# Performance work log

Hardware: AMD Instinct MI355X
Metric: run time of the kernel (lower is better)

The kernel has to match this reference:

```python
import jax, jax.numpy as jnp
import numpy as np

BS, N, F, R, OUT = 8, 512, 512, 16, 512
ALPHA = 0.2

def setup_inputs() -> dict:
    key = jax.random.key(0)
    ks = jax.random.split(key, 16)
    w = lambda k, shp: (jax.random.normal(k, shp, dtype=jnp.float32) * 0.05)
    return {
        'x_ori': jax.random.normal(ks[0], (BS, N, F), dtype=jnp.float32),
        'x': jax.random.normal(ks[1], (BS, N, F), dtype=jnp.float32),
        'c': jax.random.normal(ks[2], (BS, 1, F), dtype=jnp.float32),
        'adj': jax.random.randint(ks[3], (BS, N, N, R), 0, 2, dtype=jnp.int32),
        'Wfc': w(ks[4], (F, F)),
        'Wdc': w(ks[5], (F, F)),
        'Wqv': w(ks[6], (2 * F, F)),
        'Wkv': w(ks[7], (2 * F, F)),
        'Wqc': w(ks[8], (F, F)),
        'Wkc': w(ks[9], (F, F)),
        'Wa': w(ks[10], (2 * F, R)),
        'Wu': w(ks[11], (2 * F, OUT)),
    }

def reference(x_ori, x, c, adj, Wfc, Wdc, Wqv, Wkv, Wqc, Wkc, Wa, Wu):
    # relation-context modulation vector m: [bs,1,F]
    m = jnp.matmul(jax.nn.elu(jnp.matmul(c, Wfc)), Wdc)
    nodes = jnp.concatenate([x, x_ori], axis=2)          # [bs,N,2F]
    xq = jnp.matmul(nodes, Wqv) * jnp.matmul(m, Wqc)     # [bs,N,F]
    xk = jnp.matmul(nodes, Wkv) * jnp.matmul(m, Wkc)     # [bs,N,F]
    # scores[b,i,j,r] = leakyrelu(xq_i . Wa[:F,r] + xk_j . Wa[F:,r])
    # (equivalent to cat([xq_i,xk_j]) @ Wa without materializing [bs,N,N,2F])
    sq = jnp.matmul(xq, Wa[:F])                          # [bs,N,R]
    sk = jnp.matmul(xk, Wa[F:])                          # [bs,N,R]
    scores = jax.nn.leaky_relu(sq[:, :, None, :] + sk[:, None, :, :], ALPHA)
    adj_f = adj.astype(scores.dtype)                     # [bs,N,N,R]
    s = jnp.sum(scores * adj_f, axis=3)                  # [bs,N,N]
    mask = jnp.sum(adj_f, axis=3) > 0
    attn = jax.nn.softmax(jnp.where(mask, s, jnp.float32(-9e15)), axis=2)
    new_x = jnp.matmul(attn, x)                          # [bs,N,F]
    return jnp.matmul(jnp.concatenate([x, new_x], axis=2), Wu)
```

## Files before the change

### kernel.cpp

```cpp
#include <hip/hip_runtime.h>
#include <hip/hip_bf16.h>
#include <cstddef>
#include <cstdint>

static constexpr int BSZ  = 8;
static constexpr int NN   = 512;
static constexpr int FF   = 512;
static constexpr int RR   = 16;
static constexpr int TWOF = 1024;

typedef __attribute__((ext_vector_type(8))) short short8;
typedef __attribute__((ext_vector_type(4))) float f32x4;

__device__ __forceinline__ ushort bf16_bits(float v) {
    union { __hip_bfloat16 h; ushort u; } cvt;
    cvt.h = __float2bfloat16(v);
    return cvt.u;
}

static constexpr size_t OFF_TB     = 0;
static constexpr size_t OFF_MB     = 16384;
static constexpr size_t OFF_MQ     = 32768;
static constexpr size_t OFF_MK     = 49152;
static constexpr size_t OFF_SQ     = 65536;
static constexpr size_t OFF_SK     = 327680;
static constexpr size_t OFF_WQET   = 589824;
static constexpr size_t OFF_WKET   = 851968;
static constexpr size_t OFF_XBF    = 5308416;
static constexpr size_t OFF_XTBF   = 9502720;
static constexpr size_t OFF_XORIBF = 13697024;
static constexpr size_t OFF_NEWXBF = 17891328;
static constexpr size_t OFF_WUT    = 22085632;
static constexpr size_t OFF_MASK   = 23134208;

__global__ __launch_bounds__(256) void k_prep(
    const float* __restrict__ x_ori, const float* __restrict__ x,
    const float* __restrict__ c, const float* __restrict__ Wfc,
    const float* __restrict__ Wu, const int* __restrict__ adj,
    ushort* __restrict__ xori_bf, ushort* __restrict__ x_bf,
    ushort* __restrict__ xT_bf, ushort* __restrict__ WuT,
    float* __restrict__ tb, ushort* __restrict__ masks)
{
    int blk = blockIdx.x;
    int t = threadIdx.x;
    if (blk < 1024) {
        int idx = blk * 256 + t;
        float4 a = ((const float4*)x_ori)[idx * 2];
        float4 b = ((const float4*)x_ori)[idx * 2 + 1];
        uint4 s;
        s.x = (uint)bf16_bits(a.x) | ((uint)bf16_bits(a.y) << 16);
        s.y = (uint)bf16_bits(a.z) | ((uint)bf16_bits(a.w) << 16);
        s.z = (uint)bf16_bits(b.x) | ((uint)bf16_bits(b.y) << 16);
        s.w = (uint)bf16_bits(b.z) | ((uint)bf16_bits(b.w) << 16);
        ((uint4*)xori_bf)[idx] = s;
    } else if (blk < 3072) {
        __shared__ float tile[32][33];
        int bb = blk - 1024;
        int f0 = (bb & 15) * 32, i0 = ((bb >> 4) & 15) * 32, b = bb >> 8;
        int c2 = (t & 15) * 2, r = t >> 4;
#pragma unroll
        for (int rr = 0; rr < 32; rr += 16) {
            int i = i0 + r + rr;
            const float* xp = &x[((size_t)b * NN + i) * FF + f0 + c2];
            float v0 = xp[0], v1 = xp[1];
            tile[r + rr][c2] = v0;
            tile[r + rr][c2 + 1] = v1;
            *(uint*)&x_bf[((size_t)b * NN + i) * FF + f0 + c2] =
                (uint)bf16_bits(v0) | ((uint)bf16_bits(v1) << 16);
        }
        __syncthreads();
#pragma unroll
        for (int ff = 0; ff < 32; ff += 16) {
            int f = f0 + r + ff;
            *(uint*)&xT_bf[((size_t)b * FF + f) * NN + i0 + c2] =
                (uint)bf16_bits(tile[c2][r + ff]) |
                ((uint)bf16_bits(tile[c2 + 1][r + ff]) << 16);
        }
    } else if (blk < 3584) {
        __shared__ float tile2[32][33];
        int bb = blk - 3072;
        int f0 = (bb & 31) * 32, o0 = (bb >> 5) * 32;
        int cc = t & 31, r0 = t >> 5;
#pragma unroll
        for (int rr = 0; rr < 32; rr += 8)
            tile2[r0 + rr][cc] = Wu[(size_t)(f0 + r0 + rr) * FF + o0 + cc];
        __syncthreads();
#pragma unroll
        for (int rr = 0; rr < 32; rr += 8)
            WuT[(size_t)(o0 + r0 + rr) * TWOF + f0 + cc] = bf16_bits(tile2[cc][r0 + rr]);
    } else if (blk < 3712) {
        __shared__ float red1[8][32];
        int bb = blk - 3584;
        int b = bb >> 4, f0 = (bb & 15) * 32;
        int f = t & 31, kq = t >> 5;
        const float* vb = c + (size_t)b * FF;
        float acc = 0.f;
        int ks = kq * 64;
#pragma unroll 8
        for (int k = ks; k < ks + 64; ++k)
            acc = fmaf(vb[k], Wfc[(size_t)k * FF + f0 + f], acc);
        red1[kq][f] = acc;
        __syncthreads();
        if (kq == 0) {
            acc += red1[1][f] + red1[2][f] + red1[3][f] + red1[4][f] +
                   red1[5][f] + red1[6][f] + red1[7][f];
            tb[(size_t)b * FF + f0 + f] = (acc > 0.f) ? acc : expm1f(acc);
        }
    } else {
        int pb = (blk - 3712) * 1024;
        const int4* a4 = (const int4*)adj;
        uint* m32 = (uint*)masks;
#pragma unroll 8
        for (int i = 0; i < 16; ++i) {
            size_t g4 = (size_t)pb * 4 + (size_t)i * 256 + t;
            int4 v = a4[g4];
            uint bits = (uint)v.x | ((uint)v.y << 1) | ((uint)v.z << 2) | ((uint)v.w << 3);
            uint mp = bits << ((t & 3) * 4);
            mp |= (uint)__shfl_xor((int)mp, 1, 64);
            mp |= (uint)__shfl_xor((int)mp, 2, 64);
            uint hi = (uint)__shfl_xor((int)mp, 4, 64);
            if ((t & 7) == 0)
                m32[(size_t)pb / 2 + i * 32 + (t >> 3)] = (mp & 0xFFFFu) | (hi << 16);
        }
    }
}

__global__ __launch_bounds__(256) void k_matvec(const float* __restrict__ vin,
                                                const float* __restrict__ W,
                                                float* __restrict__ vout) {
    __shared__ float red[8][32];
    int b = blockIdx.y;
    int f0 = blockIdx.x * 32;
    int t = threadIdx.x;
    int f = t & 31, kq = t >> 5;
    const float* vb = vin + (size_t)b * FF;
    float acc = 0.f;
    int ks = kq * 64;
#pragma unroll 8
    for (int k = ks; k < ks + 64; ++k)
        acc = fmaf(vb[k], W[(size_t)k * FF + f0 + f], acc);
    red[kq][f] = acc;
    __syncthreads();
    if (kq == 0) {
        acc += red[1][f] + red[2][f] + red[3][f] + red[4][f] +
               red[5][f] + red[6][f] + red[7][f];
        vout[(size_t)b * FF + f0 + f] = acc;
    }
}

__global__ __launch_bounds__(256) void k_mqk(const float* __restrict__ m,
                                             const float* __restrict__ Wqc,
                                             const float* __restrict__ Wkc,
                                             float* __restrict__ mq,
                                             float* __restrict__ mk) {
    __shared__ float redq[8][32];
    __shared__ float redk[8][32];
    int b = blockIdx.y;
    int f0 = blockIdx.x * 32;
    int t = threadIdx.x;
    int f = t & 31, kq = t >> 5;
    const float* mb = m + (size_t)b * FF;
    float aq = 0.f, ak = 0.f;
    int ks = kq * 64;
#pragma unroll 8
    for (int k = ks; k < ks + 64; ++k) {
        float mv = mb[k];
        aq = fmaf(mv, Wqc[(size_t)k * FF + f0 + f], aq);
        ak = fmaf(mv, Wkc[(size_t)k * FF + f0 + f], ak);
    }
    redq[kq][f] = aq;
    redk[kq][f] = ak;
    __syncthreads();
    if (kq == 0) {
        aq += redq[1][f] + redq[2][f] + redq[3][f] + redq[4][f] +
              redq[5][f] + redq[6][f] + redq[7][f];
        ak += redk[1][f] + redk[2][f] + redk[3][f] + redk[4][f] +
              redk[5][f] + redk[6][f] + redk[7][f];
        mq[(size_t)b * FF + f0 + f] = aq;
        mk[(size_t)b * FF + f0 + f] = ak;
    }
}

__global__ __launch_bounds__(256) void k_weff(const float* __restrict__ Wqv,
                                              const float* __restrict__ Wkv,
                                              const float* __restrict__ Wa,
                                              const float* __restrict__ mqv,
                                              const float* __restrict__ mkv,
                                              ushort* __restrict__ WqEt,
                                              ushort* __restrict__ WkEt) {
    int z = blockIdx.z;
    const float* W = z ? Wkv : Wqv;
    const float* mvec = z ? mkv : mqv;
    ushort* WeffT = z ? WkEt : WqEt;
    int waRowOff = z ? FF : 0;

    __shared__ float4 wa4[FF * 4];
    int tid = threadIdx.x;
    int b = blockIdx.y;
    const float* mv = mvec + (size_t)b * FF;
#pragma unroll
    for (int qq = 0; qq < 8; ++qq) {
        int idx = tid + qq * 256;
        int f = idx >> 2, rq = idx & 3;
        float4 w = *reinterpret_cast<const float4*>(Wa + (size_t)(waRowOff + f) * RR + rq * 4);
        float s = mv[f];
        float4 o;
        o.x = w.x * s; o.y = w.y * s; o.z = w.z * s; o.w = w.w * s;
        wa4[idx] = o;
    }
    __syncthreads();
    int k_l = tid >> 2, r4 = tid & 3;
    int k = blockIdx.x * 64 + k_l;
    const float4* Wrow4 = reinterpret_cast<const float4*>(W + (size_t)k * FF);
    float4 acc = {0.f, 0.f, 0.f, 0.f};
#pragma unroll 4
    for (int f4 = 0; f4 < FF / 4; ++f4) {
        float4 w = Wrow4[f4];
        float4 v0 = wa4[(f4 * 4 + 0) * 4 + r4];
        float4 v1 = wa4[(f4 * 4 + 1) * 4 + r4];
        float4 v2 = wa4[(f4 * 4 + 2) * 4 + r4];
        float4 v3 = wa4[(f4 * 4 + 3) * 4 + r4];
        acc.x = fmaf(w.x, v0.x, acc.x); acc.y = fmaf(w.x, v0.y, acc.y);
        acc.z = fmaf(w.x, v0.z, acc.z); acc.w = fmaf(w.x, v0.w, acc.w);
        acc.x = fmaf(w.y, v1.x, acc.x); acc.y = fmaf(w.y, v1.y, acc.y);
        acc.z = fmaf(w.y, v1.z, acc.z); acc.w = fmaf(w.y, v1.w, acc.w);
        acc.x = fmaf(w.z, v2.x, acc.x); acc.y = fmaf(w.z, v2.y, acc.y);
        acc.z = fmaf(w.z, v2.z, acc.z); acc.w = fmaf(w.z, v2.w, acc.w);
        acc.x = fmaf(w.w, v3.x, acc.x); acc.y = fmaf(w.w, v3.y, acc.y);
        acc.z = fmaf(w.w, v3.z, acc.z); acc.w = fmaf(w.w, v3.w, acc.w);
    }
    WeffT[((size_t)b * RR + r4 * 4 + 0) * TWOF + k] = bf16_bits(acc.x);
    WeffT[((size_t)b * RR + r4 * 4 + 1) * TWOF + k] = bf16_bits(acc.y);
    WeffT[((size_t)b * RR + r4 * 4 + 2) * TWOF + k] = bf16_bits(acc.z);
    WeffT[((size_t)b * RR + r4 * 4 + 3) * TWOF + k] = bf16_bits(acc.w);
}

__global__ __launch_bounds__(256) void k_sqsk(const ushort* __restrict__ x_bf,
                                              const ushort* __restrict__ xori_bf,
                                              const ushort* __restrict__ WqEt,
                                              const ushort* __restrict__ WkEt,
                                              float* __restrict__ sq,
                                              float* __restrict__ sk) {
    int t = threadIdx.x;
    int b = blockIdx.y;
    int m0 = blockIdx.x * 32;
    int lane = t & 63, w = t >> 6;
    int sub = w & 1, isK = w >> 1;
    int m_l = lane & 15, q = lane >> 4;
    int row = m0 + sub * 16 + m_l;
    const ushort* Bt = (isK ? WkEt : WqEt) + ((size_t)b * RR + m_l) * TWOF;
    f32x4 acc = {0.f, 0.f, 0.f, 0.f};
#pragma unroll
    for (int k0 = 0; k0 < TWOF; k0 += 32) {
        const ushort* src = (k0 < FF) ? x_bf : xori_bf;
        int kc = k0 & (FF - 1);
        short8 af = *(const short8*)(src + ((size_t)b * NN + row) * FF + kc + q * 8);
        short8 bf = *(const short8*)(Bt + k0 + q * 8);
        acc = __builtin_amdgcn_mfma_f32_16x16x32_bf16(af, bf, acc, 0, 0, 0);
    }
    float* dst = isK ? sk : sq;
#pragma unroll
    for (int r = 0; r < 4; ++r) {
        int i = m0 + sub * 16 + q * 4 + r;
        dst[((size_t)b * NN + i) * RR + m_l] = acc[r];
    }
}

__global__ __launch_bounds__(256, 2) void k_attn_pv(const ushort* __restrict__ masks,
                                                    const float* __restrict__ sq,
                                                    const float* __restrict__ sk,
                                                    const ushort* __restrict__ xT_bf,
                                                    ushort* __restrict__ newx_bf) {
    constexpr int ZS = 520;
    __shared__ ushort P[16 * ZS];
    __shared__ float  sk_t[16 * NN];
    __shared__ ushort mask_lds[8 * NN];
    __shared__ float  rowsum[8];
    int t = threadIdx.x;
    int b = blockIdx.y;
    int m0 = blockIdx.x * 8;

    {
        const uint4* mg = (const uint4*)(masks + ((size_t)b * NN + m0) * NN);
        uint4* ml = (uint4*)mask_lds;
        ml[t] = mg[t];
        ml[t + 256] = mg[t + 256];
        const float4* skg = (const float4*)(sk + (size_t)b * NN * RR);
#pragma unroll
        for (int qq = 0; qq < 8; ++qq) {
            int idx = t + qq * 256;
            float4 v = skg[idx];
            int j = idx >> 2, rr = (idx & 3) * 4;
            sk_t[(rr + 0) * NN + j] = v.x;
            sk_t[(rr + 1) * NN + j] = v.y;
            sk_t[(rr + 2) * NN + j] = v.z;
            sk_t[(rr + 3) * NN + j] = v.w;
        }
        uint* pz = (uint*)&P[8 * ZS];
        for (int idx = t; idx < (8 * ZS) / 2; idx += 256) pz[idx] = 0u;
    }
    __syncthreads();

    {
        int r = t >> 5, cc = t & 31;
        int i = m0 + r;
        const float4* sqp = (const float4*)(sq + ((size_t)b * NN + i) * RR);
        float4 q0 = sqp[0], q1 = sqp[1], q2 = sqp[2], q3 = sqp[3];
        float sv[16] = {q0.x, q0.y, q0.z, q0.w, q1.x, q1.y, q1.z, q1.w,
                        q2.x, q2.y, q2.z, q2.w, q3.x, q3.y, q3.z, q3.w};
        float z[16];
#pragma unroll
        for (int it = 0; it < 16; ++it) {
            int j = it * 32 + cc;
            uint mk = mask_lds[r * NN + j];
            float ssum = 0.f;
#pragma unroll
            for (int ridx = 0; ridx < 16; ++ridx) {
                float v_ = sv[ridx] + sk_t[ridx * NN + j];
                v_ = fmaxf(v_, 0.2f * v_);
                ssum = fmaf(v_, (float)((mk >> ridx) & 1u), ssum);
            }
            z[it] = mk ? ssum : -9e15f;
        }
        float mx = z[0];
#pragma unroll
        for (int it = 1; it < 16; ++it) mx = fmaxf(mx, z[it]);
#pragma unroll
        for (int off = 1; off < 32; off <<= 1) mx = fmaxf(mx, __shfl_xor(mx, off, 32));
        float sum = 0.f;
        ushort* pr = &P[r * ZS];
#pragma unroll
        for (int it = 0; it < 16; ++it) {
            float e = __expf(z[it] - mx);
            pr[it * 32 + cc] = bf16_bits(e);
            sum += e;
        }
#pragma unroll
        for (int off = 1; off < 32; off <<= 1) sum += __shfl_xor(sum, off, 32);
        if (cc == 0) rowsum[r] = sum;
    }
    __syncthreads();

    {
        int w = t >> 6, lane = t & 63;
        int m_l = lane & 15, q = lane >> 4;
        int n0w = w * 128;
        f32x4 acc[8] = {};
        const ushort* xTb = xT_bf + (size_t)b * FF * NN;
        for (int k0 = 0; k0 < NN; k0 += 32) {
            short8 af = *(const short8*)(&P[m_l * ZS + k0 + q * 8]);
#pragma unroll
            for (int nb = 0; nb < 8; ++nb) {
                int n = n0w + nb * 16 + m_l;
                short8 bfr = *(const short8*)(xTb + (size_t)n * NN + k0 + q * 8);
                acc[nb] = __builtin_amdgcn_mfma_f32_16x16x32_bf16(af, bfr, acc[nb], 0, 0, 0);
            }
        }
        if (q < 2) {
            float inv[4];
#pragma unroll
            for (int rg = 0; rg < 4; ++rg) inv[rg] = 1.f / rowsum[q * 4 + rg];
#pragma unroll
            for (int nb = 0; nb < 8; ++nb) {
#pragma unroll
                for (int rg = 0; rg < 4; ++rg) {
                    int i = m0 + q * 4 + rg;
                    int f = n0w + nb * 16 + m_l;
                    newx_bf[((size_t)b * NN + i) * FF + f] = bf16_bits(acc[nb][rg] * inv[rg]);
                }
            }
        }
    }
}

__global__ __launch_bounds__(256) void k_gemm(const ushort* __restrict__ A1, size_t sA1,
                                              const ushort* __restrict__ A2, size_t sA2,
                                              const ushort* __restrict__ BT, size_t sBT,
                                              float* __restrict__ Cf, size_t sC,
                                              int K, int ldBT) {
    __shared__ ushort As[2][64 * 40];
    __shared__ ushort Bs[2][64 * 40];
    int t = threadIdx.x;
    int n0 = blockIdx.x * 64, m0 = blockIdx.y * 64, b = blockIdx.z;
    int row = t >> 2, c8 = (t & 3) * 8;
    int lane = t & 63, w = t >> 6;
    int m_l = lane & 15, q = lane >> 4;
    f32x4 acc[4] = {{0.f,0.f,0.f,0.f},{0.f,0.f,0.f,0.f},{0.f,0.f,0.f,0.f},{0.f,0.f,0.f,0.f}};
    const ushort* BTb = BT + (size_t)b * sBT;
    for (int k0 = 0; k0 < K; k0 += 64) {
#pragma unroll
        for (int h = 0; h < 2; ++h) {
            int kk = k0 + h * 32;
            const ushort* Aab; int kc;
            if (kk < FF) { Aab = A1 + (size_t)b * sA1; kc = kk; }
            else         { Aab = A2 + (size_t)b * sA2; kc = kk - FF; }
            uint4 av = *(const uint4*)(Aab + (size_t)(m0 + row) * FF + kc + c8);
            uint4 bv = *(const uint4*)(BTb + (size_t)(n0 + row) * ldBT + kk + c8);
            *(uint4*)(&As[h][row * 40 + c8]) = av;
            *(uint4*)(&Bs[h][row * 40 + c8]) = bv;
        }
        __syncthreads();
#pragma unroll
        for (int h = 0; h < 2; ++h) {
            short8 af = *(const short8*)(&As[h][(w * 16 + m_l) * 40 + q * 8]);
#pragma unroll
            for (int nb = 0; nb < 4; ++nb) {
                short8 bfr = *(const short8*)(&Bs[h][(nb * 16 + m_l) * 40 + q * 8]);
                acc[nb] = __builtin_amdgcn_mfma_f32_16x16x32_bf16(af, bfr, acc[nb], 0, 0, 0);
            }
        }
        __syncthreads();
    }
#pragma unroll
    for (int nb = 0; nb < 4; ++nb) {
#pragma unroll
        for (int r = 0; r < 4; ++r) {
            int mi = m0 + w * 16 + q * 4 + r;
            int ni = n0 + nb * 16 + m_l;
            Cf[(size_t)b * sC + (size_t)mi * FF + ni] = acc[nb][r];
        }
    }
}

extern "C" void kernel_launch(void* const* d_in, const int* in_sizes, int n_in,
                              void* d_out, int out_size, void* d_ws, size_t ws_size,
                              hipStream_t stream) {
    const float* x_ori = (const float*)d_in[0];
    const float* x     = (const float*)d_in[1];
    const float* c     = (const float*)d_in[2];
    const int*   adj   = (const int*)d_in[3];
    const float* Wfc   = (const float*)d_in[4];
    const float* Wdc   = (const float*)d_in[5];
    const float* Wqv   = (const float*)d_in[6];
    const float* Wkv   = (const float*)d_in[7];
    const float* Wqc   = (const float*)d_in[8];
    const float* Wkc   = (const float*)d_in[9];
    const float* Wa    = (const float*)d_in[10];
    const float* Wu    = (const float*)d_in[11];
    float* out = (float*)d_out;

    char* ws = (char*)d_ws;
    float*  tb      = (float*)(ws + OFF_TB);
    float*  mb      = (float*)(ws + OFF_MB);
    float*  mq      = (float*)(ws + OFF_MQ);
    float*  mk      = (float*)(ws + OFF_MK);
    float*  sq      = (float*)(ws + OFF_SQ);
    float*  sk      = (float*)(ws + OFF_SK);
    ushort* WqEt    = (ushort*)(ws + OFF_WQET);
    ushort* WkEt    = (ushort*)(ws + OFF_WKET);
    ushort* x_bf    = (ushort*)(ws + OFF_XBF);
    ushort* xT_bf   = (ushort*)(ws + OFF_XTBF);
    ushort* xori_bf = (ushort*)(ws + OFF_XORIBF);
    ushort* newx_bf = (ushort*)(ws + OFF_NEWXBF);
    ushort* WuT     = (ushort*)(ws + OFF_WUT);
    ushort* masks   = (ushort*)(ws + OFF_MASK);

    dim3 blk(256);

    k_prep<<<dim3(5760), blk, 0, stream>>>(x_ori, x, c, Wfc, Wu, adj,
                                           xori_bf, x_bf, xT_bf, WuT, tb, masks);

    k_matvec<<<dim3(16, BSZ), blk, 0, stream>>>(tb, Wdc, mb);
    k_mqk<<<dim3(16, BSZ), blk, 0, stream>>>(mb, Wqc, Wkc, mq, mk);

    k_weff<<<dim3(16, BSZ, 2), blk, 0, stream>>>(Wqv, Wkv, Wa, mq, mk, WqEt, WkEt);

    k_sqsk<<<dim3(16, BSZ), blk, 0, stream>>>(x_bf, xori_bf, WqEt, WkEt, sq, sk);

    k_attn_pv<<<dim3(64, BSZ), blk, 0, stream>>>(masks, sq, sk, xT_bf, newx_bf);

    k_gemm<<<dim3(8, 8, BSZ), blk, 0, stream>>>(
        x_bf, (size_t)NN * FF, newx_bf, (size_t)NN * FF,
        WuT, (size_t)0, out, (size_t)NN * FF, TWOF, TWOF);
}
```

Baseline: 327.8 us.

## Fuse adjacency mask packing into attention kernel and double rows per block

Removes the separate adjacency-to-bitmask pass from the prep kernel, so the attention kernel now reads the int32 adj tensor directly and packs the masks into LDS itself. Each block now handles 16 query rows instead of 8, which fills the full 16-row MFMA tile that was previously half zero-padded, and it reads sk straight from global memory instead of staging a transposed copy in LDS. This avoids writing and rereading the mask buffer and halves the number of blocks. The trade-off is that only 256 blocks remain, each streaming 512 KB of adj with limited parallelism, which risks bandwidth underuse on a large GPU.

```diff
diff --git a/kernel.cpp b/kernel.cpp
--- a/kernel.cpp
+++ b/kernel.cpp
@@ -31,15 +31,14 @@
 static constexpr size_t OFF_XORIBF = 13697024;
 static constexpr size_t OFF_NEWXBF = 17891328;
 static constexpr size_t OFF_WUT    = 22085632;
-static constexpr size_t OFF_MASK   = 23134208;
 
 __global__ __launch_bounds__(256) void k_prep(
     const float* __restrict__ x_ori, const float* __restrict__ x,
     const float* __restrict__ c, const float* __restrict__ Wfc,
-    const float* __restrict__ Wu, const int* __restrict__ adj,
+    const float* __restrict__ Wu,
     ushort* __restrict__ xori_bf, ushort* __restrict__ x_bf,
     ushort* __restrict__ xT_bf, ushort* __restrict__ WuT,
-    float* __restrict__ tb, ushort* __restrict__ masks)
+    float* __restrict__ tb)
 {
     int blk = blockIdx.x;
     int t = threadIdx.x;
@@ -88,7 +87,7 @@
 #pragma unroll
         for (int rr = 0; rr < 32; rr += 8)
             WuT[(size_t)(o0 + r0 + rr) * TWOF + f0 + cc] = bf16_bits(tile2[cc][r0 + rr]);
-    } else if (blk < 3712) {
+    } else {
         __shared__ float red1[8][32];
         int bb = blk - 3584;
         int b = bb >> 4, f0 = (bb & 15) * 32;
@@ -105,22 +104,6 @@
             acc += red1[1][f] + red1[2][f] + red1[3][f] + red1[4][f] +
                    red1[5][f] + red1[6][f] + red1[7][f];
             tb[(size_t)b * FF + f0 + f] = (acc > 0.f) ? acc : expm1f(acc);
-        }
-    } else {
-        int pb = (blk - 3712) * 1024;
-        const int4* a4 = (const int4*)adj;
-        uint* m32 = (uint*)masks;
-#pragma unroll 8
-        for (int i = 0; i < 16; ++i) {
-            size_t g4 = (size_t)pb * 4 + (size_t)i * 256 + t;
-            int4 v = a4[g4];
-            uint bits = (uint)v.x | ((uint)v.y << 1) | ((uint)v.z << 2) | ((uint)v.w << 3);
-            uint mp = bits << ((t & 3) * 4);
-            mp |= (uint)__shfl_xor((int)mp, 1, 64);
-            mp |= (uint)__shfl_xor((int)mp, 2, 64);
-            uint hi = (uint)__shfl_xor((int)mp, 4, 64);
-            if ((t & 7) == 0)
-                m32[(size_t)pb / 2 + i * 32 + (t >> 3)] = (mp & 0xFFFFu) | (hi << 16);
         }
     }
 }
@@ -266,57 +249,58 @@
     }
 }
 
-__global__ __launch_bounds__(256, 2) void k_attn_pv(const ushort* __restrict__ masks,
+__global__ __launch_bounds__(256, 2) void k_attn_pv(const int* __restrict__ adj,
                                                     const float* __restrict__ sq,
                                                     const float* __restrict__ sk,
                                                     const ushort* __restrict__ xT_bf,
                                                     ushort* __restrict__ newx_bf) {
     constexpr int ZS = 520;
     __shared__ ushort P[16 * ZS];
-    __shared__ float  sk_t[16 * NN];
-    __shared__ ushort mask_lds[8 * NN];
-    __shared__ float  rowsum[8];
+    __shared__ ushort mask_lds[16 * NN];
+    __shared__ float  rowsum[16];
     int t = threadIdx.x;
     int b = blockIdx.y;
-    int m0 = blockIdx.x * 8;
+    int m0 = blockIdx.x * 16;
 
     {
-        const uint4* mg = (const uint4*)(masks + ((size_t)b * NN + m0) * NN);
-        uint4* ml = (uint4*)mask_lds;
-        ml[t] = mg[t];
-        ml[t + 256] = mg[t + 256];
-        const float4* skg = (const float4*)(sk + (size_t)b * NN * RR);
-#pragma unroll
-        for (int qq = 0; qq < 8; ++qq) {
-            int idx = t + qq * 256;
-            float4 v = skg[idx];
-            int j = idx >> 2, rr = (idx & 3) * 4;
-            sk_t[(rr + 0) * NN + j] = v.x;
-            sk_t[(rr + 1) * NN + j] = v.y;
-            sk_t[(rr + 2) * NN + j] = v.z;
-            sk_t[(rr + 3) * NN + j] = v.w;
-        }
-        uint* pz = (uint*)&P[8 * ZS];
-        for (int idx = t; idx < (8 * ZS) / 2; idx += 256) pz[idx] = 0u;
+        const int4* a4 = (const int4*)adj + ((size_t)b * NN + m0) * (NN * RR / 4);
+        uint* ml = (uint*)mask_lds;
+#pragma unroll 8
+        for (int it = 0; it < 128; ++it) {
+            int4 v = a4[it * 256 + t];
+            uint bits = (uint)v.x | ((uint)v.y << 1) | ((uint)v.z << 2) | ((uint)v.w << 3);
+            uint mp = bits << ((t & 3) * 4);
+            mp |= (uint)__shfl_xor((int)mp, 1, 64);
+            mp |= (uint)__shfl_xor((int)mp, 2, 64);
+            uint hi = (uint)__shfl_xor((int)mp, 4, 64);
+            if ((t & 7) == 0) {
+                int p = (it * 256 + t) >> 2;
+                ml[p >> 1] = (mp & 0xFFFFu) | (hi << 16);
+            }
+        }
     }
     __syncthreads();
 
     {
-        int r = t >> 5, cc = t & 31;
+        int r = t >> 4, cc = t & 15;
         int i = m0 + r;
         const float4* sqp = (const float4*)(sq + ((size_t)b * NN + i) * RR);
         float4 q0 = sqp[0], q1 = sqp[1], q2 = sqp[2], q3 = sqp[3];
         float sv[16] = {q0.x, q0.y, q0.z, q0.w, q1.x, q1.y, q1.z, q1.w,
                         q2.x, q2.y, q2.z, q2.w, q3.x, q3.y, q3.z, q3.w};
-        float z[16];
-#pragma unroll
-        for (int it = 0; it < 16; ++it) {
-            int j = it * 32 + cc;
+        float z[32];
+#pragma unroll 4
+        for (int it = 0; it < 32; ++it) {
+            int j = it * 16 + cc;
             uint mk = mask_lds[r * NN + j];
+            const float4* kp = (const float4*)(sk + ((size_t)b * NN + j) * RR);
+            float4 s0 = kp[0], s1 = kp[1], s2 = kp[2], s3 = kp[3];
+            float ks[16] = {s0.x, s0.y, s0.z, s0.w, s1.x, s1.y, s1.z, s1.w,
+                            s2.x, s2.y, s2.z, s2.w, s3.x, s3.y, s3.z, s3.w};
             float ssum = 0.f;
 #pragma unroll
             for (int ridx = 0; ridx < 16; ++ridx) {
-                float v_ = sv[ridx] + sk_t[ridx * NN + j];
+                float v_ = sv[ridx] + ks[ridx];
                 v_ = fmaxf(v_, 0.2f * v_);
                 ssum = fmaf(v_, (float)((mk >> ridx) & 1u), ssum);
             }
@@ -324,19 +308,19 @@
         }
         float mx = z[0];
 #pragma unroll
-        for (int it = 1; it < 16; ++it) mx = fmaxf(mx, z[it]);
-#pragma unroll
-        for (int off = 1; off < 32; off <<= 1) mx = fmaxf(mx, __shfl_xor(mx, off, 32));
+        for (int it = 1; it < 32; ++it) mx = fmaxf(mx, z[it]);
+#pragma unroll
+        for (int off = 1; off < 16; off <<= 1) mx = fmaxf(mx, __shfl_xor(mx, off, 64));
         float sum = 0.f;
         ushort* pr = &P[r * ZS];
 #pragma unroll
-        for (int it = 0; it < 16; ++it) {
+        for (int it = 0; it < 32; ++it) {
             float e = __expf(z[it] - mx);
-            pr[it * 32 + cc] = bf16_bits(e);
+            pr[it * 16 + cc] = bf16_bits(e);
             sum += e;
         }
 #pragma unroll
-        for (int off = 1; off < 32; off <<= 1) sum += __shfl_xor(sum, off, 32);
+        for (int off = 1; off < 16; off <<= 1) sum += __shfl_xor(sum, off, 64);
         if (cc == 0) rowsum[r] = sum;
     }
     __syncthreads();
@@ -356,18 +340,16 @@
                 acc[nb] = __builtin_amdgcn_mfma_f32_16x16x32_bf16(af, bfr, acc[nb], 0, 0, 0);
             }
         }
-        if (q < 2) {
-            float inv[4];
-#pragma unroll
-            for (int rg = 0; rg < 4; ++rg) inv[rg] = 1.f / rowsum[q * 4 + rg];
-#pragma unroll
-            for (int nb = 0; nb < 8; ++nb) {
-#pragma unroll
-                for (int rg = 0; rg < 4; ++rg) {
-                    int i = m0 + q * 4 + rg;
-                    int f = n0w + nb * 16 + m_l;
-                    newx_bf[((size_t)b * NN + i) * FF + f] = bf16_bits(acc[nb][rg] * inv[rg]);
-                }
+        float inv[4];
+#pragma unroll
+        for (int rg = 0; rg < 4; ++rg) inv[rg] = 1.f / rowsum[q * 4 + rg];
+#pragma unroll
+        for (int nb = 0; nb < 8; ++nb) {
+#pragma unroll
+            for (int rg = 0; rg < 4; ++rg) {
+                int i = m0 + q * 4 + rg;
+                int f = n0w + nb * 16 + m_l;
+                newx_bf[((size_t)b * NN + i) * FF + f] = bf16_bits(acc[nb][rg] * inv[rg]);
             }
         }
     }
@@ -453,12 +435,11 @@
     ushort* xori_bf = (ushort*)(ws + OFF_XORIBF);
     ushort* newx_bf = (ushort*)(ws + OFF_NEWXBF);
     ushort* WuT     = (ushort*)(ws + OFF_WUT);
-    ushort* masks   = (ushort*)(ws + OFF_MASK);
 
     dim3 blk(256);
 
-    k_prep<<<dim3(5760), blk, 0, stream>>>(x_ori, x, c, Wfc, Wu, adj,
-                                           xori_bf, x_bf, xT_bf, WuT, tb, masks);
+    k_prep<<<dim3(3712), blk, 0, stream>>>(x_ori, x, c, Wfc, Wu,
+                                           xori_bf, x_bf, xT_bf, WuT, tb);
 
     k_matvec<<<dim3(16, BSZ), blk, 0, stream>>>(tb, Wdc, mb);
     k_mqk<<<dim3(16, BSZ), blk, 0, stream>>>(mb, Wqc, Wkc, mq, mk);
@@ -467,7 +448,7 @@
 
     k_sqsk<<<dim3(16, BSZ), blk, 0, stream>>>(x_bf, xori_bf, WqEt, WkEt, sq, sk);
 
-    k_attn_pv<<<dim3(64, BSZ), blk, 0, stream>>>(masks, sq, sk, xT_bf, newx_bf);
+    k_attn_pv<<<dim3(32, BSZ), blk, 0, stream>>>(adj, sq, sk, xT_bf, newx_bf);
 
     k_gemm<<<dim3(8, 8, BSZ), blk, 0, stream>>>(
         x_bf, (size_t)NN * FF, newx_bf, (size_t)NN * FF,
```

New measurement: 362.3 us. 1.11x slower.
